# Kernel optimization log

Measured on AMD Instinct MI355X. Metric: run time of the kernel, lower is better.

The kernel has to match this reference:

```python
import jax, jax.numpy as jnp
import numpy as np

B_PAIR = 4      # anchor/positive pairs; total batch = 2*B_PAIR
NUM = 4096      # keypoints per cloud
C_FEAT = 640    # descriptor dim
NB_ITER = 5


def _rigid_transform(a, b, weights):
    # a: (B,M,3), b: (B,M,3), weights: (B,M) -> (B,3,4)
    wn = weights[..., None] / (jnp.sum(weights[..., None], axis=1, keepdims=True) + 1e-5)
    centroid_a = jnp.sum(a * wn, axis=1)            # (B,3)
    centroid_b = jnp.sum(b * wn, axis=1)
    a_c = a - centroid_a[:, None, :]
    b_c = b - centroid_b[:, None, :]
    cov = jnp.swapaxes(a_c, -2, -1) @ (b_c * wn)    # (B,3,3)
    u, s, vh = jnp.linalg.svd(cov, full_matrices=False)
    v = jnp.swapaxes(vh, -2, -1)                    # torch.svd returns v, jax returns vh
    rot_pos = v @ jnp.swapaxes(u, -2, -1)
    v_neg = v.at[:, :, 2].multiply(-1.0)
    rot_neg = v_neg @ jnp.swapaxes(u, -2, -1)
    rot = jnp.where(jnp.linalg.det(rot_pos)[:, None, None] > 0, rot_pos, rot_neg)
    trans = -rot @ centroid_a[:, :, None] + centroid_b[:, :, None]
    return jnp.concatenate((rot, trans), axis=2)    # (B,3,4)


def _uot_forward(point_features, point_coords, gamma, epsilon):
    feats = point_features[..., 0]                  # (2B, C, N)
    twoB, _, N = feats.shape
    B = twoB // 2
    feat1 = jnp.transpose(feats[:B], (0, 2, 1))     # (B, N, C)
    feat2 = jnp.transpose(feats[B:], (0, 2, 1))
    coords = point_coords.reshape(twoB, -1, 4)
    coords1 = coords[:B, :, 1:]                     # (B, N, 3)
    coords2 = coords[B:, :, 1:]

    eps = jnp.exp(epsilon) + 0.03                   # scalar (1,)
    gam = jnp.exp(gamma)

    f1 = feat1 / jnp.sqrt(jnp.sum(feat1**2, -1, keepdims=True) + 1e-8)
    f2 = feat2 / jnp.sqrt(jnp.sum(feat2**2, -1, keepdims=True) + 1e-8)
    Cmat = 1.0 - jnp.einsum('bnc,bmc->bnm', f1, f2)  # (B,N,N) cosine cost
    K = jnp.exp(-Cmat / eps)

    power = gam / (gam + eps)
    inv_n = jnp.asarray(1.0 / N, K.dtype)
    a = jnp.full((B, N, 1), inv_n, K.dtype)
    prob1 = jnp.full((B, N, 1), inv_n, K.dtype)
    prob2 = jnp.full((B, N, 1), inv_n, K.dtype)
    b = prob2
    for _ in range(NB_ITER):                        # unrolled unbalanced Sinkhorn
        KTa = jnp.matmul(jnp.swapaxes(K, 1, 2), a)  # (B,N,1)
        b = jnp.power(prob2 / (KTa + 1e-8), power)
        Kb = jnp.matmul(K, b)
        a = jnp.power(prob1 / (Kb + 1e-8), power)
    T = a * K * jnp.swapaxes(b, 1, 2)               # (B,N,N) transport plan

    row_sum = jnp.sum(T, axis=-1, keepdims=True)    # (B,N,1)
    sinkhorn_matches = jnp.matmul(T, coords2) / (row_sum + 1e-8)  # (B,N,3)
    transform = _rigid_transform(coords1, sinkhorn_matches, row_sum[..., 0])
    return T, sinkhorn_matches, transform


def setup_inputs() -> dict:
    key = jax.random.key(0)
    k1, k2 = jax.random.split(key)
    point_features = jax.random.normal(k1, (2 * B_PAIR, C_FEAT, NUM, 1), dtype=jnp.float32)
    point_coords = jax.random.normal(k2, (2 * B_PAIR * NUM, 4), dtype=jnp.float32) * 10.0
    gamma = jnp.zeros((1,), jnp.float32)
    epsilon = jnp.zeros((1,), jnp.float32)
    return {"point_features": point_features, "point_coords": point_coords,
            "gamma": gamma, "epsilon": epsilon}


def reference(point_features, point_coords, gamma, epsilon):
    return _uot_forward(point_features, point_coords, gamma, epsilon)
```

## Files before the change

### kernel.cpp

```cpp
#include <hip/hip_runtime.h>
#include <math.h>

#define NB 4
#define N 4096
#define CF 640

typedef _Float16 f16;
typedef _Float16 f16x8 __attribute__((ext_vector_type(8)));
typedef _Float16 f16x4 __attribute__((ext_vector_type(4)));
typedef float    f32x4 __attribute__((ext_vector_type(4)));
typedef unsigned int u32;

#define OFF_FNT   0ll
#define OFF_RNORM (OFF_FNT + 8ll*N*CF*2)
#define OFF_BVEC  (OFF_RNORM + 8ll*N*4)
#define OFF_SCR   (OFF_BVEC + (long long)NB*N*4)
#define OFF_KTAP  (OFF_SCR + (long long)NB*N*N*2)
#define REQ_H     (OFF_KTAP + (long long)NB*64*N*4)
#define REQ_F     (OFF_SCR + (long long)NB*64*N*4)

__device__ inline void async_copy16(void* lds, const void* g) {
    __builtin_amdgcn_global_load_lds(
        (const __attribute__((address_space(1))) u32*)g,
        (__attribute__((address_space(3))) u32*)lds,
        16, 0, 0);
}

__global__ __launch_bounds__(256) void rnorm_kernel(const float* __restrict__ pf,
                                                    float* __restrict__ rnorm) {
    int idx = blockIdx.x * 256 + threadIdx.x;
    int n = idx & (N - 1);
    int b = idx >> 12;
    const float* src = pf + (size_t)b * CF * N + n;
    float s = 0.f;
    for (int c = 0; c < CF; ++c) { float v = src[(size_t)c * N]; s = fmaf(v, v, s); }
    rnorm[idx] = 1.0f / sqrtf(s + 1e-8f);
}

__global__ __launch_bounds__(256) void transpose_kernel(const float* __restrict__ pf,
                                                        const float* __restrict__ rnorm,
                                                        f16* __restrict__ fnT) {
    __shared__ float tile[64][65];
    int b  = blockIdx.z;
    int c0 = blockIdx.x * 64;
    int n1 = blockIdx.y * 64;
    int t  = threadIdx.x;

    int c_l = t >> 4;
    int n_l4 = (t & 15) * 4;
    #pragma unroll
    for (int i = 0; i < 4; ++i) {
        int c = c_l + i * 16;
        float4 v = *(const float4*)(pf + (size_t)(b * CF + c0 + c) * N + n1 + n_l4);
        tile[c][n_l4 + 0] = v.x; tile[c][n_l4 + 1] = v.y;
        tile[c][n_l4 + 2] = v.z; tile[c][n_l4 + 3] = v.w;
    }
    __syncthreads();

    int n_l = t >> 2;
    int c_g = (t & 3) * 16;
    float rn = rnorm[b * N + n1 + n_l];
    f16 tmp[16] __attribute__((aligned(16)));
    #pragma unroll
    for (int i = 0; i < 16; ++i)
        tmp[i] = (f16)(tile[c_g + i][n_l] * rn);
    f16* dst = fnT + (size_t)(b * N + n1 + n_l) * CF + c0 + c_g;
    ((uint4*)dst)[0] = ((const uint4*)tmp)[0];
    ((uint4*)dst)[1] = ((const uint4*)tmp)[1];
}

template<bool H>
__global__ __launch_bounds__(256) void gemm_k(const f16* __restrict__ fnT,
                                              const float* __restrict__ e_in,
                                              float* __restrict__ Kf,
                                              f16* __restrict__ Kh,
                                              float* __restrict__ ktap) {
    int b  = blockIdx.z;
    int m0 = blockIdx.y * 128;
    int n0 = blockIdx.x * 128;
    const f16* A = fnT + (size_t)b       * N * CF;
    const f16* B = fnT + (size_t)(b + 4) * N * CF;

    __shared__ f16 As[128 * 32];
    __shared__ f16 Bs[128 * 32];
    __shared__ float cs[2][128];
    __shared__ f16 Ct[H ? 128 * 136 : 1];

    int tid = threadIdx.x;
    int w = tid >> 6;
    int l = tid & 63;
    int wr = w >> 1, wc = w & 1;

    f32x4 acc[4][4];
    #pragma unroll
    for (int i = 0; i < 4; ++i)
        #pragma unroll
        for (int j = 0; j < 4; ++j)
            acc[i][j] = (f32x4){0.f, 0.f, 0.f, 0.f};

    int srow = l >> 2;
    int scp  = l & 3;

    for (int c0 = 0; c0 < CF; c0 += 32) {
        #pragma unroll
        for (int q = 0; q < 2; ++q) {
            int ch = w * 2 + q;
            int row = ch * 16 + srow;
            int cc = scp ^ ((row >> 1) & 3);
            async_copy16(&As[ch * 512], A + (size_t)(n0 + row) * CF + c0 + cc * 8);
            async_copy16(&Bs[ch * 512], B + (size_t)(m0 + row) * CF + c0 + cc * 8);
        }
        __syncthreads();

        f16x8 af[4], bfr[4];
        int g = l >> 4, low = l & 15;
        #pragma unroll
        for (int t = 0; t < 4; ++t) {
            int rowA = wr * 64 + t * 16 + low;
            af[t] = *(const f16x8*)(As + rowA * 32 + (g ^ ((rowA >> 1) & 3)) * 8);
            int rowB = wc * 64 + t * 16 + low;
            bfr[t] = *(const f16x8*)(Bs + rowB * 32 + (g ^ ((rowB >> 1) & 3)) * 8);
        }
        #pragma unroll
        for (int i = 0; i < 4; ++i)
            #pragma unroll
            for (int j = 0; j < 4; ++j)
                acc[i][j] = __builtin_amdgcn_mfma_f32_16x16x32_f16(af[i], bfr[j], acc[i][j], 0, 0, 0);
        __syncthreads();
    }

    float eps = expf(e_in[0]) + 0.03f;
    float inv_eps = 1.0f / eps;
    int g4 = l >> 4, low = l & 15;
    float colp[4] = {0.f, 0.f, 0.f, 0.f};
    float* out = Kf + (size_t)b * N * N;

    #pragma unroll
    for (int i = 0; i < 4; ++i) {
        int rl = wr * 64 + i * 16 + g4 * 4;
        #pragma unroll
        for (int j = 0; j < 4; ++j) {
            int cl = wc * 64 + j * 16 + low;
            #pragma unroll
            for (int r = 0; r < 4; ++r) {
                float v = expf((acc[i][j][r] - 1.0f) * inv_eps);
                out[(size_t)(n0 + rl + r) * N + m0 + cl] = v;
                if constexpr (H) Ct[(rl + r) * 136 + cl] = (f16)v;
                colp[j] += v;
            }
        }
    }

    #pragma unroll
    for (int j = 0; j < 4; ++j) {
        float c = colp[j];
        c += __shfl_down(c, 32);
        c += __shfl_down(c, 16);
        if (l < 16) cs[wr][wc * 64 + j * 16 + l] = c;
    }
    __syncthreads();
    if (tid < 128)
        ktap[((size_t)b * 64 + blockIdx.x) * N + m0 + tid] =
            (cs[0][tid] + cs[1][tid]) * (1.0f / N);

    if constexpr (H) {
        f16* oh = Kh + (size_t)b * N * N;
        int row0 = tid >> 4, c8 = (tid & 15) * 8;
        #pragma unroll
        for (int rr = 0; rr < 8; ++rr) {
            int row = rr * 16 + row0;
            f16x8 v = *(const f16x8*)(Ct + row * 136 + c8);
            *(f16x8*)(oh + (size_t)(n0 + row) * N + m0 + c8) = v;
        }
    }
}

__global__ __launch_bounds__(256) void bvec_kernel(const float* __restrict__ ktap, int npart,
                                                   const float* __restrict__ g_in,
                                                   const float* __restrict__ e_in,
                                                   float* __restrict__ bvec) {
    int i = blockIdx.x * 256 + threadIdx.x;
    int b = i >> 12, m = i & (N - 1);
    const float* p = ktap + (size_t)b * 64 * N + m;
    float s = 0.f;
    for (int k = 0; k < npart; ++k) s += p[(size_t)k * N];
    float eps = expf(e_in[0]) + 0.03f;
    float gam = expf(g_in[0]);
    float power = gam / (gam + eps);
    bvec[i] = powf((1.0f / N) / (s + 1e-8f), power);
}

template<bool H>
__global__ __launch_bounds__(256) void fused_iter(const void* __restrict__ Kp,
                                                  const float* __restrict__ bv_in,
                                                  const float* __restrict__ g_in,
                                                  const float* __restrict__ e_in,
                                                  float* __restrict__ ktap) {
    int b = blockIdx.y, slab = blockIdx.x;
    int n0s = slab * 64;
    int w = threadIdx.x >> 6, l = threadIdx.x & 63;
    __shared__ float ash[64];
    float eps = expf(e_in[0]) + 0.03f;
    float gam = expf(g_in[0]);
    float power = gam / (gam + eps);
    const float* bv = bv_in + b * N;

    float acc[16];
    #pragma unroll
    for (int q = 0; q < 16; ++q) acc[q] = 0.f;

    if constexpr (H) {
        const f16* Kb = (const f16*)Kp + ((size_t)b * N + n0s) * N;
        for (int it = 0; it < 8; ++it) {
            int m = it * 512 + l * 8;
            float bq[8];
            *(float4*)&bq[0] = *(const float4*)(bv + m);
            *(float4*)&bq[4] = *(const float4*)(bv + m + 4);
            #pragma unroll
            for (int rr = 0; rr < 16; ++rr) {
                f16x8 v = *(const f16x8*)(Kb + (size_t)(rr * 4 + w) * N + m);
                #pragma unroll
                for (int q = 0; q < 8; ++q) acc[rr] = fmaf((float)v[q], bq[q], acc[rr]);
            }
        }
    } else {
        const float* Kb = (const float*)Kp + ((size_t)b * N + n0s) * N;
        for (int it = 0; it < 16; ++it) {
            int m = it * 256 + l * 4;
            float4 bq = *(const float4*)(bv + m);
            #pragma unroll
            for (int rr = 0; rr < 16; ++rr) {
                float4 v = *(const float4*)(Kb + (size_t)(rr * 4 + w) * N + m);
                acc[rr] = fmaf(v.x, bq.x, acc[rr]);
                acc[rr] = fmaf(v.y, bq.y, acc[rr]);
                acc[rr] = fmaf(v.z, bq.z, acc[rr]);
                acc[rr] = fmaf(v.w, bq.w, acc[rr]);
            }
        }
    }
    #pragma unroll
    for (int rr = 0; rr < 16; ++rr) {
        float s = acc[rr];
        s += __shfl_down(s, 32);
        s += __shfl_down(s, 16);
        s += __shfl_down(s, 8);
        s += __shfl_down(s, 4);
        s += __shfl_down(s, 2);
        s += __shfl_down(s, 1);
        if (l == 0) ash[rr * 4 + w] = powf((1.0f / N) / (s + 1e-8f), power);
    }
    __syncthreads();

    float cacc[16];
    #pragma unroll
    for (int q = 0; q < 16; ++q) cacc[q] = 0.f;
    int t4 = threadIdx.x * 4;
    if constexpr (H) {
        const f16* Kb = (const f16*)Kp + ((size_t)b * N + n0s) * N;
        for (int r = 0; r < 64; ++r) {
            float a = ash[r];
            #pragma unroll
            for (int q = 0; q < 4; ++q) {
                f16x4 v = *(const f16x4*)(Kb + (size_t)r * N + q * 1024 + t4);
                #pragma unroll
                for (int j = 0; j < 4; ++j)
                    cacc[q * 4 + j] = fmaf((float)v[j], a, cacc[q * 4 + j]);
            }
        }
    } else {
        const float* Kb = (const float*)Kp + ((size_t)b * N + n0s) * N;
        for (int r = 0; r < 64; ++r) {
            float a = ash[r];
            #pragma unroll
            for (int q = 0; q < 4; ++q) {
                float4 v = *(const float4*)(Kb + (size_t)r * N + q * 1024 + t4);
                cacc[q * 4 + 0] = fmaf(v.x, a, cacc[q * 4 + 0]);
                cacc[q * 4 + 1] = fmaf(v.y, a, cacc[q * 4 + 1]);
                cacc[q * 4 + 2] = fmaf(v.z, a, cacc[q * 4 + 2]);
                cacc[q * 4 + 3] = fmaf(v.w, a, cacc[q * 4 + 3]);
            }
        }
    }
    float* o = ktap + ((size_t)b * 64 + slab) * N;
    #pragma unroll
    for (int q = 0; q < 4; ++q)
        *(float4*)(o + q * 1024 + t4) =
            make_float4(cacc[q * 4], cacc[q * 4 + 1], cacc[q * 4 + 2], cacc[q * 4 + 3]);
}

__global__ __launch_bounds__(256) void final_k(float* __restrict__ Tout,
                                               const float* __restrict__ bv_in,
                                               const float* __restrict__ g_in,
                                               const float* __restrict__ e_in,
                                               const float* __restrict__ pc,
                                               float* __restrict__ rowsum,
                                               float* __restrict__ matches) {
    int b = blockIdx.y, n = blockIdx.x;
    int t = threadIdx.x;
    int t4 = t * 4;
    const float* bv = bv_in + b * N;
    float kv[16], bl[16];
    float* Trow = Tout + ((size_t)b * N + n) * N;
    #pragma unroll
    for (int q = 0; q < 4; ++q) {
        *(float4*)&bl[q * 4] = *(const float4*)(bv + q * 1024 + t4);
        *(float4*)&kv[q * 4] = *(const float4*)(Trow + q * 1024 + t4);
    }
    float s = 0.f;
    #pragma unroll
    for (int q = 0; q < 16; ++q) s = fmaf(kv[q], bl[q], s);
    __shared__ float red[256];
    red[t] = s; __syncthreads();
    for (int off = 128; off; off >>= 1) {
        if (t < off) red[t] += red[t + off];
        __syncthreads();
    }
    __shared__ float a_sh;
    if (t == 0) {
        float eps = expf(e_in[0]) + 0.03f;
        float gam = expf(g_in[0]);
        float power = gam / (gam + eps);
        a_sh = powf((1.0f / N) / (red[0] + 1e-8f), power);
    }
    __syncthreads();
    float an = a_sh;
    const float4* c2 = (const float4*)pc + (size_t)(4 + b) * N;
    float rs = 0.f, s0 = 0.f, s1 = 0.f, s2 = 0.f;
    #pragma unroll
    for (int q = 0; q < 4; ++q) {
        float tv0 = an * kv[q * 4 + 0] * bl[q * 4 + 0];
        float tv1 = an * kv[q * 4 + 1] * bl[q * 4 + 1];
        float tv2 = an * kv[q * 4 + 2] * bl[q * 4 + 2];
        float tv3 = an * kv[q * 4 + 3] * bl[q * 4 + 3];
        *(float4*)(Trow + q * 1024 + t4) = make_float4(tv0, tv1, tv2, tv3);
        rs += tv0 + tv1 + tv2 + tv3;
        float4 c0 = c2[q * 1024 + t4],     c1 = c2[q * 1024 + t4 + 1],
               cc = c2[q * 1024 + t4 + 2], c3 = c2[q * 1024 + t4 + 3];
        s0 = fmaf(tv0, c0.y, s0); s1 = fmaf(tv0, c0.z, s1); s2 = fmaf(tv0, c0.w, s2);
        s0 = fmaf(tv1, c1.y, s0); s1 = fmaf(tv1, c1.z, s1); s2 = fmaf(tv1, c1.w, s2);
        s0 = fmaf(tv2, cc.y, s0); s1 = fmaf(tv2, cc.z, s1); s2 = fmaf(tv2, cc.w, s2);
        s0 = fmaf(tv3, c3.y, s0); s1 = fmaf(tv3, c3.z, s1); s2 = fmaf(tv3, c3.w, s2);
    }
    __shared__ float4 red4[256];
    red4[t] = make_float4(rs, s0, s1, s2); __syncthreads();
    for (int off = 128; off; off >>= 1) {
        if (t < off) {
            float4 o = red4[t + off];
            red4[t].x += o.x; red4[t].y += o.y; red4[t].z += o.z; red4[t].w += o.w;
        }
        __syncthreads();
    }
    if (t == 0) {
        float4 tot = red4[0];
        rowsum[b * N + n] = tot.x;
        float inv = 1.0f / (tot.x + 1e-8f);
        float* mo = matches + ((size_t)b * N + n) * 3;
        mo[0] = tot.y * inv; mo[1] = tot.z * inv; mo[2] = tot.w * inv;
    }
}

__global__ __launch_bounds__(256) void transform_kernel(const float* __restrict__ rowsum,
                                                        const float* __restrict__ matches,
                                                        const float* __restrict__ pc,
                                                        float* __restrict__ out) {
    int b = blockIdx.x;
    float vals[16];
    #pragma unroll
    for (int q = 0; q < 16; ++q) vals[q] = 0.f;
    for (int n = threadIdx.x; n < N; n += 256) {
        float w = rowsum[b * N + n];
        float4 c1 = ((const float4*)pc)[(size_t)b * N + n];
        float ax = c1.y, ay = c1.z, az = c1.w;
        const float* mm = matches + ((size_t)b * N + n) * 3;
        float bx = mm[0], by = mm[1], bz = mm[2];
        vals[0] += w;
        vals[1] = fmaf(w, ax, vals[1]); vals[2] = fmaf(w, ay, vals[2]); vals[3] = fmaf(w, az, vals[3]);
        vals[4] = fmaf(w, bx, vals[4]); vals[5] = fmaf(w, by, vals[5]); vals[6] = fmaf(w, bz, vals[6]);
        vals[7]  = fmaf(w * ax, bx, vals[7]);  vals[8]  = fmaf(w * ax, by, vals[8]);  vals[9]  = fmaf(w * ax, bz, vals[9]);
        vals[10] = fmaf(w * ay, bx, vals[10]); vals[11] = fmaf(w * ay, by, vals[11]); vals[12] = fmaf(w * ay, bz, vals[12]);
        vals[13] = fmaf(w * az, bx, vals[13]); vals[14] = fmaf(w * az, by, vals[14]); vals[15] = fmaf(w * az, bz, vals[15]);
    }
    __shared__ float red[256];
    __shared__ float tot[16];
    for (int q = 0; q < 16; ++q) {
        red[threadIdx.x] = vals[q]; __syncthreads();
        for (int off = 128; off; off >>= 1) {
            if (threadIdx.x < off) red[threadIdx.x] += red[threadIdx.x + off];
            __syncthreads();
        }
        if (threadIdx.x == 0) tot[q] = red[0];
        __syncthreads();
    }
    if (threadIdx.x != 0) return;

    double S = tot[0];
    double denom = S + 1e-5;
    double Ca[3], Cb[3], M[3][3], cov[3][3];
    for (int i = 0; i < 3; ++i) { Ca[i] = tot[1 + i] / denom; Cb[i] = tot[4 + i] / denom; }
    for (int i = 0; i < 3; ++i)
        for (int j = 0; j < 3; ++j)
            M[i][j] = tot[7 + i * 3 + j] / denom;
    double s0 = S / denom;
    for (int i = 0; i < 3; ++i)
        for (int j = 0; j < 3; ++j)
            cov[i][j] = M[i][j] - Ca[i] * Cb[j] * (2.0 - s0);

    double Sm[3][3], V[3][3] = {{1,0,0},{0,1,0},{0,0,1}};
    for (int i = 0; i < 3; ++i)
        for (int j = 0; j < 3; ++j) {
            double acc = 0;
            for (int k = 0; k < 3; ++k) acc += cov[k][i] * cov[k][j];
            Sm[i][j] = acc;
        }
    for (int sweep = 0; sweep < 20; ++sweep) {
        static const int pq[3][2] = {{0,1},{0,2},{1,2}};
        for (int r = 0; r < 3; ++r) {
            int p = pq[r][0], q = pq[r][1];
            double apq = Sm[p][q];
            if (fabs(apq) < 1e-30) continue;
            double tau = (Sm[q][q] - Sm[p][p]) / (2.0 * apq);
            double t = (tau >= 0) ? 1.0 / (tau + sqrt(1.0 + tau * tau))
                                  : 1.0 / (tau - sqrt(1.0 + tau * tau));
            double c = 1.0 / sqrt(1.0 + t * t), s = t * c;
            for (int i = 0; i < 3; ++i) {
                double sip = Sm[i][p], siq = Sm[i][q];
                Sm[i][p] = c * sip - s * siq; Sm[i][q] = s * sip + c * siq;
            }
            for (int j = 0; j < 3; ++j) {
                double spj = Sm[p][j], sqj = Sm[q][j];
                Sm[p][j] = c * spj - s * sqj; Sm[q][j] = s * spj + c * sqj;
            }
            for (int i = 0; i < 3; ++i) {
                double vip = V[i][p], viq = V[i][q];
                V[i][p] = c * vip - s * viq; V[i][q] = s * vip + c * viq;
            }
        }
    }
    double lam[3] = {Sm[0][0], Sm[1][1], Sm[2][2]};
    for (int i = 0; i < 2; ++i)
        for (int j = i + 1; j < 3; ++j)
            if (lam[j] > lam[i]) {
                double tl = lam[i]; lam[i] = lam[j]; lam[j] = tl;
                for (int k = 0; k < 3; ++k) { double tv = V[k][i]; V[k][i] = V[k][j]; V[k][j] = tv; }
            }
    double U[3][3];
    double sig0 = sqrt(fmax(lam[0], 0.0));
    for (int j = 0; j < 3; ++j) {
        double sig = sqrt(fmax(lam[j], 0.0));
        if (sig > 1e-12 * (sig0 + 1e-300)) {
            double nrm = 0;
            for (int i = 0; i < 3; ++i) {
                double u = cov[i][0] * V[0][j] + cov[i][1] * V[1][j] + cov[i][2] * V[2][j];
                U[i][j] = u; nrm += u * u;
            }
            nrm = 1.0 / sqrt(nrm + 1e-300);
            for (int i = 0; i < 3; ++i) U[i][j] *= nrm;
        } else {
            U[0][j] = U[1][0] * U[2][1] - U[2][0] * U[1][1];
            U[1][j] = U[2][0] * U[0][1] - U[0][0] * U[2][1];
            U[2][j] = U[0][0] * U[1][1] - U[1][0] * U[0][1];
        }
    }
    double R[3][3];
    for (int i = 0; i < 3; ++i)
        for (int j = 0; j < 3; ++j)
            R[i][j] = V[i][0] * U[j][0] + V[i][1] * U[j][1] + V[i][2] * U[j][2];
    double det = R[0][0] * (R[1][1] * R[2][2] - R[1][2] * R[2][1])
               - R[0][1] * (R[1][0] * R[2][2] - R[1][2] * R[2][0])
               + R[0][2] * (R[1][0] * R[2][1] - R[1][1] * R[2][0]);
    if (!(det > 0)) {
        for (int k = 0; k < 3; ++k) V[k][2] = -V[k][2];
        for (int i = 0; i < 3; ++i)
            for (int j = 0; j < 3; ++j)
                R[i][j] = V[i][0] * U[j][0] + V[i][1] * U[j][1] + V[i][2] * U[j][2];
    }
    double tr[3];
    for (int i = 0; i < 3; ++i)
        tr[i] = -(R[i][0] * Ca[0] + R[i][1] * Ca[1] + R[i][2] * Ca[2]) + Cb[i];
    float* o = out + b * 12;
    for (int i = 0; i < 3; ++i) {
        o[i * 4 + 0] = (float)R[i][0];
        o[i * 4 + 1] = (float)R[i][1];
        o[i * 4 + 2] = (float)R[i][2];
        o[i * 4 + 3] = (float)tr[i];
    }
}

extern "C" void kernel_launch(void* const* d_in, const int* in_sizes, int n_in,
                              void* d_out, int out_size, void* d_ws, size_t ws_size,
                              hipStream_t stream) {
    const float* pf   = (const float*)d_in[0];
    const float* pc   = (const float*)d_in[1];
    const float* g_in = (const float*)d_in[2];
    const float* e_in = (const float*)d_in[3];

    char* wsb = (char*)d_ws;
    f16*   fnT   = (f16*)(wsb + OFF_FNT);
    float* rnorm = (float*)(wsb + OFF_RNORM);
    float* bvec  = (float*)(wsb + OFF_BVEC);

    float* T_out   = (float*)d_out;
    float* matches = T_out + (size_t)NB * N * N;
    float* trans   = matches + (size_t)NB * N * 3;
    float* rowsum  = rnorm;

    rnorm_kernel<<<dim3(8 * N / 256), 256, 0, stream>>>(pf, rnorm);
    transpose_kernel<<<dim3(CF / 64, N / 64, 8), 256, 0, stream>>>(pf, rnorm, fnT);

    if (ws_size >= (size_t)REQ_H) {
        f16*   Kh   = (f16*)(wsb + OFF_SCR);
        float* ktap = (float*)(wsb + OFF_KTAP);
        gemm_k<true><<<dim3(N / 128, N / 128, NB), 256, 0, stream>>>(fnT, e_in, T_out, Kh, ktap);
        bvec_kernel<<<dim3(NB * N / 256), 256, 0, stream>>>(ktap, 32, g_in, e_in, bvec);
        for (int it = 0; it < 4; ++it) {
            fused_iter<true><<<dim3(64, NB), 256, 0, stream>>>(Kh, bvec, g_in, e_in, ktap);
            bvec_kernel<<<dim3(NB * N / 256), 256, 0, stream>>>(ktap, 64, g_in, e_in, bvec);
        }
        final_k<<<dim3(N, NB), 256, 0, stream>>>(T_out, bvec, g_in, e_in, pc, rowsum, matches);
    } else {
        float* ktap = (float*)(wsb + OFF_SCR);
        gemm_k<false><<<dim3(N / 128, N / 128, NB), 256, 0, stream>>>(fnT, e_in, T_out, (f16*)nullptr, ktap);
        bvec_kernel<<<dim3(NB * N / 256), 256, 0, stream>>>(ktap, 32, g_in, e_in, bvec);
        for (int it = 0; it < 4; ++it) {
            fused_iter<false><<<dim3(64, NB), 256, 0, stream>>>(T_out, bvec, g_in, e_in, ktap);
            bvec_kernel<<<dim3(NB * N / 256), 256, 0, stream>>>(ktap, 64, g_in, e_in, bvec);
        }
        final_k<<<dim3(N, NB), 256, 0, stream>>>(T_out, bvec, g_in, e_in, pc, rowsum, matches);
    }

    transform_kernel<<<dim3(NB), 256, 0, stream>>>(rowsum, matches, pc, trans);
}
```

Baseline: 996.8 us.

## Shrink Sinkhorn iteration slabs to 16 rows and parallelize partial-sum reduction

Each fused Sinkhorn iteration block now handles 16 rows instead of 64, so the grid has 256 slabs per batch instead of 64 (1024 blocks versus 256) and fills the GPU's compute units better. Each block still writes one column partial of length N, so there are now 256 partials per batch. These are stored in the reused feature-transpose workspace region. The bvec reduction kernel splits the partial sum across four waves and combines them through shared memory. The trade-off is four times more partial-sum traffic for the reduction kernel to read.

After: 867.6 us. -13.0%, faster.

```diff
diff --git a/kernel.cpp b/kernel.cpp
--- a/kernel.cpp
+++ b/kernel.cpp
@@ -175,19 +175,29 @@
     }
 }
 
-__global__ __launch_bounds__(256) void bvec_kernel(const float* __restrict__ ktap, int npart,
+__global__ __launch_bounds__(256) void bvec_kernel(const float* __restrict__ ktap,
+                                                   int npart, int slotstride,
                                                    const float* __restrict__ g_in,
                                                    const float* __restrict__ e_in,
                                                    float* __restrict__ bvec) {
-    int i = blockIdx.x * 256 + threadIdx.x;
+    int cl = threadIdx.x & 63;
+    int pg = threadIdx.x >> 6;
+    int i = blockIdx.x * 64 + cl;
     int b = i >> 12, m = i & (N - 1);
-    const float* p = ktap + (size_t)b * 64 * N + m;
+    const float* p = ktap + (size_t)b * slotstride * N + m;
+    int per = npart >> 2;
     float s = 0.f;
-    for (int k = 0; k < npart; ++k) s += p[(size_t)k * N];
-    float eps = expf(e_in[0]) + 0.03f;
-    float gam = expf(g_in[0]);
-    float power = gam / (gam + eps);
-    bvec[i] = powf((1.0f / N) / (s + 1e-8f), power);
+    #pragma unroll 8
+    for (int k = pg * per; k < (pg + 1) * per; ++k) s += p[(size_t)k * N];
+    __shared__ float sh[4][64];
+    sh[pg][cl] = s; __syncthreads();
+    if (threadIdx.x < 64) {
+        float tot = sh[0][cl] + sh[1][cl] + sh[2][cl] + sh[3][cl];
+        float eps = expf(e_in[0]) + 0.03f;
+        float gam = expf(g_in[0]);
+        float power = gam / (gam + eps);
+        bvec[i] = powf((1.0f / N) / (tot + 1e-8f), power);
+    }
 }
 
 template<bool H>
@@ -197,17 +207,15 @@
                                                   const float* __restrict__ e_in,
                                                   float* __restrict__ ktap) {
     int b = blockIdx.y, slab = blockIdx.x;
-    int n0s = slab * 64;
+    int n0s = slab * 16;
     int w = threadIdx.x >> 6, l = threadIdx.x & 63;
-    __shared__ float ash[64];
+    __shared__ float ash[16];
     float eps = expf(e_in[0]) + 0.03f;
     float gam = expf(g_in[0]);
     float power = gam / (gam + eps);
     const float* bv = bv_in + b * N;
 
-    float acc[16];
-    #pragma unroll
-    for (int q = 0; q < 16; ++q) acc[q] = 0.f;
+    float acc[4] = {0.f, 0.f, 0.f, 0.f};
 
     if constexpr (H) {
         const f16* Kb = (const f16*)Kp + ((size_t)b * N + n0s) * N;
@@ -217,8 +225,8 @@
             *(float4*)&bq[0] = *(const float4*)(bv + m);
             *(float4*)&bq[4] = *(const float4*)(bv + m + 4);
             #pragma unroll
-            for (int rr = 0; rr < 16; ++rr) {
-                f16x8 v = *(const f16x8*)(Kb + (size_t)(rr * 4 + w) * N + m);
+            for (int rr = 0; rr < 4; ++rr) {
+                f16x8 v = *(const f16x8*)(Kb + (size_t)(w * 4 + rr) * N + m);
                 #pragma unroll
                 for (int q = 0; q < 8; ++q) acc[rr] = fmaf((float)v[q], bq[q], acc[rr]);
             }
@@ -229,7 +237,7 @@
             int m = it * 256 + l * 4;
             float4 bq = *(const float4*)(bv + m);
             #pragma unroll
-            for (int rr = 0; rr < 16; ++rr) {
+            for (int rr = 0; rr < 4; ++rr) {
                 float4 v = *(const float4*)(Kb + (size_t)(rr * 4 + w) * N + m);
                 acc[rr] = fmaf(v.x, bq.x, acc[rr]);
                 acc[rr] = fmaf(v.y, bq.y, acc[rr]);
@@ -239,7 +247,7 @@
         }
     }
     #pragma unroll
-    for (int rr = 0; rr < 16; ++rr) {
+    for (int rr = 0; rr < 4; ++rr) {
         float s = acc[rr];
         s += __shfl_down(s, 32);
         s += __shfl_down(s, 16);
@@ -247,7 +255,8 @@
         s += __shfl_down(s, 4);
         s += __shfl_down(s, 2);
         s += __shfl_down(s, 1);
-        if (l == 0) ash[rr * 4 + w] = powf((1.0f / N) / (s + 1e-8f), power);
+        if (l == 0) ash[(H ? w * 4 + rr : rr * 4 + w)] =
+            powf((1.0f / N) / (s + 1e-8f), power);
     }
     __syncthreads();
 
@@ -257,7 +266,7 @@
     int t4 = threadIdx.x * 4;
     if constexpr (H) {
         const f16* Kb = (const f16*)Kp + ((size_t)b * N + n0s) * N;
-        for (int r = 0; r < 64; ++r) {
+        for (int r = 0; r < 16; ++r) {
             float a = ash[r];
             #pragma unroll
             for (int q = 0; q < 4; ++q) {
@@ -269,7 +278,7 @@
         }
     } else {
         const float* Kb = (const float*)Kp + ((size_t)b * N + n0s) * N;
-        for (int r = 0; r < 64; ++r) {
+        for (int r = 0; r < 16; ++r) {
             float a = ash[r];
             #pragma unroll
             for (int q = 0; q < 4; ++q) {
@@ -281,7 +290,7 @@
             }
         }
     }
-    float* o = ktap + ((size_t)b * 64 + slab) * N;
+    float* o = ktap + ((size_t)b * 256 + slab) * N;
     #pragma unroll
     for (int q = 0; q < 4; ++q)
         *(float4*)(o + q * 1024 + t4) =
@@ -507,23 +516,25 @@
     rnorm_kernel<<<dim3(8 * N / 256), 256, 0, stream>>>(pf, rnorm);
     transpose_kernel<<<dim3(CF / 64, N / 64, 8), 256, 0, stream>>>(pf, rnorm, fnT);
 
+    float* ktapF = (float*)(wsb + OFF_FNT);
+
     if (ws_size >= (size_t)REQ_H) {
-        f16*   Kh   = (f16*)(wsb + OFF_SCR);
-        float* ktap = (float*)(wsb + OFF_KTAP);
-        gemm_k<true><<<dim3(N / 128, N / 128, NB), 256, 0, stream>>>(fnT, e_in, T_out, Kh, ktap);
-        bvec_kernel<<<dim3(NB * N / 256), 256, 0, stream>>>(ktap, 32, g_in, e_in, bvec);
+        f16*   Kh    = (f16*)(wsb + OFF_SCR);
+        float* ktapG = (float*)(wsb + OFF_KTAP);
+        gemm_k<true><<<dim3(N / 128, N / 128, NB), 256, 0, stream>>>(fnT, e_in, T_out, Kh, ktapG);
+        bvec_kernel<<<dim3(NB * N / 64), 256, 0, stream>>>(ktapG, 32, 64, g_in, e_in, bvec);
         for (int it = 0; it < 4; ++it) {
-            fused_iter<true><<<dim3(64, NB), 256, 0, stream>>>(Kh, bvec, g_in, e_in, ktap);
-            bvec_kernel<<<dim3(NB * N / 256), 256, 0, stream>>>(ktap, 64, g_in, e_in, bvec);
+            fused_iter<true><<<dim3(N / 16, NB), 256, 0, stream>>>(Kh, bvec, g_in, e_in, ktapF);
+            bvec_kernel<<<dim3(NB * N / 64), 256, 0, stream>>>(ktapF, 256, 256, g_in, e_in, bvec);
         }
         final_k<<<dim3(N, NB), 256, 0, stream>>>(T_out, bvec, g_in, e_in, pc, rowsum, matches);
     } else {
-        float* ktap = (float*)(wsb + OFF_SCR);
-        gemm_k<false><<<dim3(N / 128, N / 128, NB), 256, 0, stream>>>(fnT, e_in, T_out, (f16*)nullptr, ktap);
-        bvec_kernel<<<dim3(NB * N / 256), 256, 0, stream>>>(ktap, 32, g_in, e_in, bvec);
+        float* ktapG = (float*)(wsb + OFF_SCR);
+        gemm_k<false><<<dim3(N / 128, N / 128, NB), 256, 0, stream>>>(fnT, e_in, T_out, (f16*)nullptr, ktapG);
+        bvec_kernel<<<dim3(NB * N / 64), 256, 0, stream>>>(ktapG, 32, 64, g_in, e_in, bvec);
         for (int it = 0; it < 4; ++it) {
-            fused_iter<false><<<dim3(64, NB), 256, 0, stream>>>(T_out, bvec, g_in, e_in, ktap);
-            bvec_kernel<<<dim3(NB * N / 256), 256, 0, stream>>>(ktap, 64, g_in, e_in, bvec);
+            fused_iter<false><<<dim3(N / 16, NB), 256, 0, stream>>>(T_out, bvec, g_in, e_in, ktapF);
+            bvec_kernel<<<dim3(NB * N / 64), 256, 0, stream>>>(ktapF, 256, 256, g_in, e_in, bvec);
         }
         final_k<<<dim3(N, NB), 256, 0, stream>>>(T_out, bvec, g_in, e_in, pc, rowsum, matches);
     }
```
